# Optimization experiments

Hardware: AMD Instinct MI355X
Metric: run time of the kernel (lower is better)

Reference implementation:

```python
import jax, jax.numpy as jnp
import numpy as np

NEG = -1e30

def setup_inputs() -> dict:
    key = jax.random.key(0)
    k1, k2, k3, k4, k5 = jax.random.split(key, 5)
    B, N, M, D = 32, 2048, 512, 512
    C = jax.random.normal(k1, (B, N, D), dtype=jnp.float32)
    Q = jax.random.normal(k2, (B, M, D), dtype=jnp.float32)
    Cmask = jax.random.randint(k3, (B, N), 0, 2, dtype=jnp.int32)
    Qmask = jax.random.randint(k4, (B, M), 0, 2, dtype=jnp.int32)
    # Linear(3*dim, 1, bias=False) weight, flattened to a (3*dim,) vector.
    bound = 1.0 / np.sqrt(3 * D)
    w = jax.random.uniform(k5, (3 * D,), dtype=jnp.float32, minval=-bound, maxval=bound)
    return {"C": C, "Q": Q, "Cmask": Cmask, "Qmask": Qmask, "w": w}

def reference(C, Q, Cmask, Qmask, w):
    D = C.shape[-1]
    w1, w2, w3 = w[:D], w[D:2 * D], w[2 * D:]
    # Trilinear similarity, decomposed: S = w1.Ct + w2.Qt + w3.(Ct*Qt)
    S = (jnp.einsum('bnd,d->bn', C, w1)[:, :, None]
         + jnp.einsum('bmd,d->bm', Q, w2)[:, None, :]
         + jnp.einsum('bnd,bmd->bnm', C * w3, Q))  # [B, N, M]
    Qm = Qmask.astype(S.dtype)[:, None, :]  # [B, 1, M]; 1 = masked
    Cm = Cmask.astype(S.dtype)[:, :, None]  # [B, N, 1]
    S1 = jax.nn.softmax(S * (1.0 - Qm) + Qm * NEG, axis=2)
    S2 = jax.nn.softmax(S * (1.0 - Cm) + Cm * NEG, axis=1)
    A = jnp.einsum('bnm,bmd->bnd', S1, Q)
    T = jnp.einsum('bnm,bnd->bmd', S2, C)     # S2^T @ C
    Bout = jnp.einsum('bnm,bmd->bnd', S1, T)  # S1 @ (S2^T @ C)
    return (A, Bout)
```

## Files before the change

kernel.cpp:

```cpp
#include <hip/hip_runtime.h>

#define BB 32
#define NN 2048
#define MM 512
#define DD 512
#define TS 64
#define KC 16
#define PAD 4
#define LDKH 40

typedef _Float16 half4f __attribute__((ext_vector_type(4)));
typedef _Float16 half8f __attribute__((ext_vector_type(8)));
typedef float    f32x16 __attribute__((ext_vector_type(16)));

__global__ __launch_bounds__(256) void k_dots(const float* __restrict__ C, const float* __restrict__ Q,
                                              const float* __restrict__ w,
                                              float* __restrict__ c1, float* __restrict__ q2) {
    int wid  = blockIdx.x * 4 + (threadIdx.x >> 6);
    int lane = threadIdx.x & 63;
    const int NR1 = BB * NN;
    const float* src; const float* wv; float* dst;
    if (wid < NR1) { src = C + (size_t)wid * DD; wv = w;       dst = c1 + wid; }
    else { int r = wid - NR1; src = Q + (size_t)r * DD; wv = w + DD; dst = q2 + r; }
    float4 a0 = *(const float4*)(src + lane * 8);
    float4 a1 = *(const float4*)(src + lane * 8 + 4);
    float4 b0 = *(const float4*)(wv  + lane * 8);
    float4 b1 = *(const float4*)(wv  + lane * 8 + 4);
    float s = a0.x * b0.x + a0.y * b0.y + a0.z * b0.z + a0.w * b0.w
            + a1.x * b1.x + a1.y * b1.y + a1.z * b1.z + a1.w * b1.w;
#pragma unroll
    for (int o = 32; o > 0; o >>= 1) s += __shfl_down(s, o);
    if (lane == 0) *dst = s;
}

__global__ __launch_bounds__(256) void k_qt(const float* __restrict__ Q, const int* __restrict__ Qmask,
                                            _Float16* __restrict__ Qt) {
    __shared__ float Ls[64][65];
    const int bid = blockIdx.x;
    const int b   = bid >> 6;
    const int rem = bid & 63;
    const int m0  = (rem >> 3) << 6;
    const int d0  = (rem & 7) << 6;
    const int tid = threadIdx.x;
    const int r   = tid >> 4;
    const int c4  = (tid & 15) << 2;
#pragma unroll
    for (int p = 0; p < 4; ++p) {
        float4 v = *(const float4*)(Q + ((size_t)(b * MM + m0 + r + p * 16)) * DD + d0 + c4);
        const int m = r + p * 16;
        Ls[c4 + 0][m] = v.x; Ls[c4 + 1][m] = v.y; Ls[c4 + 2][m] = v.z; Ls[c4 + 3][m] = v.w;
    }
    __syncthreads();
    float z[4];
#pragma unroll
    for (int i = 0; i < 4; ++i) z[i] = Qmask[b * MM + m0 + c4 + i] ? 0.f : 1.f;
#pragma unroll
    for (int p = 0; p < 4; ++p) {
        const int d = r + p * 16;
        half4f o;
#pragma unroll
        for (int i = 0; i < 4; ++i) o[i] = (_Float16)(Ls[d][c4 + i] * z[i]);
        *(half4f*)&Qt[((size_t)(b * DD + d0 + d)) * MM + m0 + c4] = o;
    }
}

__global__ __launch_bounds__(256) void k_ct(const float* __restrict__ C, _Float16* __restrict__ Ct) {
    __shared__ float Ls[64][65];
    const int bid = blockIdx.x;
    const int b   = bid >> 8;
    const int nn0 = ((bid >> 3) & 31) << 6;
    const int dd0 = (bid & 7) << 6;
    const int tid = threadIdx.x;
    const int r   = tid >> 4;
    const int c4  = (tid & 15) << 2;
#pragma unroll
    for (int p = 0; p < 4; ++p) {
        const int n = r + (p << 4);
        float4 v = *(const float4*)(C + ((size_t)(b * NN + nn0 + n)) * DD + dd0 + c4);
        Ls[c4 + 0][n] = v.x; Ls[c4 + 1][n] = v.y; Ls[c4 + 2][n] = v.z; Ls[c4 + 3][n] = v.w;
    }
    __syncthreads();
#pragma unroll
    for (int p = 0; p < 4; ++p) {
        const int d = r + (p << 4);
        half4f o;
#pragma unroll
        for (int i = 0; i < 4; ++i) o[i] = (_Float16)Ls[d][c4 + i];
        *(half4f*)&Ct[((size_t)(b * DD + dd0 + d)) * NN + nn0 + c4] = o;
    }
}

__global__ __launch_bounds__(256) void k_te(const _Float16* __restrict__ E, const int* __restrict__ Cmask,
                                            _Float16* __restrict__ Et) {
    __shared__ float Ls[64][65];
    const int bid = blockIdx.x;
    const int b   = bid >> 8;
    const int nn0 = ((bid >> 3) & 31) << 6;
    const int mm0 = (bid & 7) << 6;
    const int tid = threadIdx.x;
    const int r   = tid >> 4;
    const int c4  = (tid & 15) << 2;
#pragma unroll
    for (int p = 0; p < 4; ++p) {
        const int n = r + (p << 4);
        half4f v = *(const half4f*)&E[((size_t)(b * NN + nn0 + n)) * MM + mm0 + c4];
        const float z = Cmask[b * NN + nn0 + n] ? 0.f : 1.f;
        Ls[c4 + 0][n] = (float)v[0] * z; Ls[c4 + 1][n] = (float)v[1] * z;
        Ls[c4 + 2][n] = (float)v[2] * z; Ls[c4 + 3][n] = (float)v[3] * z;
    }
    __syncthreads();
#pragma unroll
    for (int p = 0; p < 4; ++p) {
        const int m = r + (p << 4);
        half4f o;
#pragma unroll
        for (int i = 0; i < 4; ++i) o[i] = (_Float16)Ls[m][c4 + i];
        *(half4f*)&Et[((size_t)(b * MM + mm0 + m)) * NN + nn0 + c4] = o;
    }
}

__global__ __launch_bounds__(256, 2) void k_sgemm(const float* __restrict__ C, const float* __restrict__ Q,
                                                  const float* __restrict__ w,
                                                  const int* __restrict__ Cmask, const int* __restrict__ Qmask,
                                                  const float* __restrict__ c1, const float* __restrict__ q2,
                                                  _Float16* __restrict__ E, float* __restrict__ rsum,
                                                  float* __restrict__ csum) {
    __shared__ _Float16 Ah[128 * LDKH], Al[128 * LDKH], Bh[128 * LDKH], Bl[128 * LDKH];
    __shared__ float rowp[128], colp[128], cmz[128], qmz[128], c1s[128], q2s[128];
    const int hw  = blockIdx.x;
    const int bid = ((hw & 7) << 8) | (hw >> 3);
    const int b   = bid >> 6;
    const int rem = bid & 63;
    const int n0  = (rem >> 2) << 7;
    const int m0  = (rem & 3) << 7;
    const int tid = threadIdx.x;
    const int lane = tid & 63;
    const int wid  = tid >> 6;
    const int wr = wid >> 1, wc = wid & 1;
    const int srow = tid >> 3;
    const int sc4  = (tid & 7) << 2;
    if (tid < 128) {
        rowp[tid] = 0.f; colp[tid] = 0.f;
        cmz[tid] = Cmask[b * NN + n0 + tid] ? 0.f : 1.f;
        c1s[tid] = c1[b * NN + n0 + tid];
    } else {
        const int t = tid - 128;
        qmz[t] = Qmask[b * MM + m0 + t] ? 0.f : 1.f;
        q2s[t] = q2[b * MM + m0 + t];
    }
    f32x16 accH[2][2] = {};
    f32x16 accX[2][2] = {};
    const int ar  = wr * 64 + (lane & 31);
    const int bc  = wc * 64 + (lane & 31);
    const int kof = (lane >> 5) << 3;
    const float* Cb = C + ((size_t)(b * NN + n0)) * DD;
    const float* Qb = Q + ((size_t)(b * MM + m0)) * DD;
    const float* w3 = w + 2 * DD;
    for (int k0 = 0; k0 < DD; k0 += 32) {
        float4 wv = *(const float4*)(w3 + k0 + sc4);
        float4 ca[4], qa[4];
#pragma unroll
        for (int p = 0; p < 4; ++p) {
            ca[p] = *(const float4*)(Cb + (size_t)(srow + (p << 5)) * DD + k0 + sc4);
            qa[p] = *(const float4*)(Qb + (size_t)(srow + (p << 5)) * DD + k0 + sc4);
        }
        __syncthreads();
#pragma unroll
        for (int p = 0; p < 4; ++p) {
            const int ofs = (srow + (p << 5)) * LDKH + sc4;
            float ax[4] = {ca[p].x * wv.x, ca[p].y * wv.y, ca[p].z * wv.z, ca[p].w * wv.w};
            float bx[4] = {qa[p].x, qa[p].y, qa[p].z, qa[p].w};
            half4f ah, al, bh, bl;
#pragma unroll
            for (int e = 0; e < 4; ++e) {
                _Float16 h = (_Float16)ax[e]; ah[e] = h;
                al[e] = (_Float16)((ax[e] - (float)h) * 2048.f);
                _Float16 g = (_Float16)bx[e]; bh[e] = g;
                bl[e] = (_Float16)((bx[e] - (float)g) * 2048.f);
            }
            *(half4f*)&Ah[ofs] = ah; *(half4f*)&Al[ofs] = al;
            *(half4f*)&Bh[ofs] = bh; *(half4f*)&Bl[ofs] = bl;
        }
        __syncthreads();
#pragma unroll
        for (int h = 0; h < 2; ++h) {
            const int ko = (h << 4) + kof;
            half8f ah0 = *(const half8f*)&Ah[ar * LDKH + ko];
            half8f ah1 = *(const half8f*)&Ah[(ar + 32) * LDKH + ko];
            half8f al0 = *(const half8f*)&Al[ar * LDKH + ko];
            half8f al1 = *(const half8f*)&Al[(ar + 32) * LDKH + ko];
            half8f bh0 = *(const half8f*)&Bh[bc * LDKH + ko];
            half8f bh1 = *(const half8f*)&Bh[(bc + 32) * LDKH + ko];
            half8f bl0 = *(const half8f*)&Bl[bc * LDKH + ko];
            half8f bl1 = *(const half8f*)&Bl[(bc + 32) * LDKH + ko];
            accH[0][0] = __builtin_amdgcn_mfma_f32_32x32x16_f16(ah0, bh0, accH[0][0], 0, 0, 0);
            accH[0][1] = __builtin_amdgcn_mfma_f32_32x32x16_f16(ah0, bh1, accH[0][1], 0, 0, 0);
            accH[1][0] = __builtin_amdgcn_mfma_f32_32x32x16_f16(ah1, bh0, accH[1][0], 0, 0, 0);
            accH[1][1] = __builtin_amdgcn_mfma_f32_32x32x16_f16(ah1, bh1, accH[1][1], 0, 0, 0);
            accX[0][0] = __builtin_amdgcn_mfma_f32_32x32x16_f16(ah0, bl0, accX[0][0], 0, 0, 0);
            accX[0][0] = __builtin_amdgcn_mfma_f32_32x32x16_f16(al0, bh0, accX[0][0], 0, 0, 0);
            accX[0][1] = __builtin_amdgcn_mfma_f32_32x32x16_f16(ah0, bl1, accX[0][1], 0, 0, 0);
            accX[0][1] = __builtin_amdgcn_mfma_f32_32x32x16_f16(al0, bh1, accX[0][1], 0, 0, 0);
            accX[1][0] = __builtin_amdgcn_mfma_f32_32x32x16_f16(ah1, bl0, accX[1][0], 0, 0, 0);
            accX[1][0] = __builtin_amdgcn_mfma_f32_32x32x16_f16(al1, bh0, accX[1][0], 0, 0, 0);
            accX[1][1] = __builtin_amdgcn_mfma_f32_32x32x16_f16(ah1, bl1, accX[1][1], 0, 0, 0);
            accX[1][1] = __builtin_amdgcn_mfma_f32_32x32x16_f16(al1, bh1, accX[1][1], 0, 0, 0);
        }
    }
    const float inv2k = 4.8828125e-4f;
    const int mcol0 = wc * 64 + (lane & 31);
    const float qz0 = qmz[mcol0], qz1 = qmz[mcol0 + 32];
    const float q2v0 = q2s[mcol0], q2v1 = q2s[mcol0 + 32];
    const int hi4 = (lane >> 5) << 2;
    float colacc0 = 0.f, colacc1 = 0.f;
#pragma unroll
    for (int i = 0; i < 2; ++i) {
#pragma unroll
        for (int r = 0; r < 16; ++r) {
            const int nloc = wr * 64 + i * 32 + (r & 3) + ((r >> 2) << 3) + hi4;
            const float base = c1s[nloc];
            float S0 = accH[i][0][r] + accX[i][0][r] * inv2k + base + q2v0;
            float S1 = accH[i][1][r] + accX[i][1][r] * inv2k + base + q2v1;
            float e0 = __expf(S0), e1 = __expf(S1);
            _Float16 h0 = (_Float16)e0, h1 = (_Float16)e1;
            float eq0 = (float)h0, eq1 = (float)h1;
            const size_t erow = ((size_t)(b * NN + n0 + nloc)) * MM + m0;
            E[erow + mcol0]      = h0;
            E[erow + mcol0 + 32] = h1;
            const float cz = cmz[nloc];
            colacc0 += eq0 * cz;
            colacc1 += eq1 * cz;
            float rv = eq0 * qz0 + eq1 * qz1;
            rv += __shfl_xor(rv, 1);  rv += __shfl_xor(rv, 2);
            rv += __shfl_xor(rv, 4);  rv += __shfl_xor(rv, 8);
            rv += __shfl_xor(rv, 16);
            if ((lane & 31) == 0) atomicAdd(&rowp[nloc], rv);
        }
    }
    atomicAdd(&colp[mcol0], colacc0);
    atomicAdd(&colp[mcol0 + 32], colacc1);
    __syncthreads();
    if (tid < 128) atomicAdd(&rsum[b * NN + n0 + tid], rowp[tid]);
    else atomicAdd(&csum[b * MM + m0 + tid - 128], colp[tid - 128]);
}

__global__ __launch_bounds__(256, 2) void k_T(const _Float16* __restrict__ Ct,
                                              const _Float16* __restrict__ Et,
                                              const float* __restrict__ csum,
                                              const int* __restrict__ Qmask,
                                              _Float16* __restrict__ Tt) {
    __shared__ _Float16 As[128 * LDKH];
    __shared__ _Float16 Bs[128 * LDKH];
    const int hw  = blockIdx.x;
    const int bid = ((hw & 7) << 6) | (hw >> 3);
    const int b   = bid >> 4;
    const int rem = bid & 15;
    const int d0  = (rem >> 2) << 7;
    const int m0  = (rem & 3) << 7;
    const int tid = threadIdx.x;
    const int lane = tid & 63;
    const int wid  = tid >> 6;
    const int wr = wid >> 1, wc = wid & 1;
    const int srow = tid >> 2;
    const int scol = (tid & 3) << 3;
    const _Float16* g0 = Ct + ((size_t)(b * DD + d0 + srow)) * NN + scol;
    const _Float16* g1 = Et + ((size_t)(b * MM + m0 + srow)) * NN + scol;
    const int wofs = srow * LDKH + scol;
    f32x16 acc[2][2] = {};
    const int ar  = wr * 64 + (lane & 31);
    const int bc  = wc * 64 + (lane & 31);
    const int kof = (lane >> 5) << 3;
    for (int k0 = 0; k0 < NN; k0 += 32) {
        half8f a0v = *(const half8f*)(g0 + k0);
        half8f a1v = *(const half8f*)(g0 + k0 + (size_t)64 * NN);
        half8f b0v = *(const half8f*)(g1 + k0);
        half8f b1v = *(const half8f*)(g1 + k0 + (size_t)64 * NN);
        __syncthreads();
        *(half8f*)&As[wofs]             = a0v;
        *(half8f*)&As[wofs + 64 * LDKH] = a1v;
        *(half8f*)&Bs[wofs]             = b0v;
        *(half8f*)&Bs[wofs + 64 * LDKH] = b1v;
        __syncthreads();
#pragma unroll
        for (int h = 0; h < 2; ++h) {
            const int ko = (h << 4) + kof;
            half8f a0 = *(const half8f*)&As[ar * LDKH + ko];
            half8f a1 = *(const half8f*)&As[(ar + 32) * LDKH + ko];
            half8f b0 = *(const half8f*)&Bs[bc * LDKH + ko];
            half8f b1 = *(const half8f*)&Bs[(bc + 32) * LDKH + ko];
            acc[0][0] = __builtin_amdgcn_mfma_f32_32x32x16_f16(a0, b0, acc[0][0], 0, 0, 0);
            acc[0][1] = __builtin_amdgcn_mfma_f32_32x32x16_f16(a0, b1, acc[0][1], 0, 0, 0);
            acc[1][0] = __builtin_amdgcn_mfma_f32_32x32x16_f16(a1, b0, acc[1][0], 0, 0, 0);
            acc[1][1] = __builtin_amdgcn_mfma_f32_32x32x16_f16(a1, b1, acc[1][1], 0, 0, 0);
        }
    }
    const int mc0 = m0 + wc * 64 + (lane & 31);
    const float s0 = (Qmask[b * MM + mc0]      ? 0.f : 1.f) / csum[b * MM + mc0];
    const float s1 = (Qmask[b * MM + mc0 + 32] ? 0.f : 1.f) / csum[b * MM + mc0 + 32];
    const int hi4 = (lane >> 5) << 2;
#pragma unroll
    for (int i = 0; i < 2; ++i) {
#pragma unroll
        for (int r = 0; r < 16; ++r) {
            const int d = d0 + wr * 64 + i * 32 + (r & 3) + ((r >> 2) << 3) + hi4;
            const size_t o = ((size_t)(b * DD + d)) * MM + mc0;
            Tt[o]      = (_Float16)(acc[i][0][r] * s0);
            Tt[o + 32] = (_Float16)(acc[i][1][r] * s1);
        }
    }
}

#define KS 32

__global__ __launch_bounds__(256, 2) void k_AB(const _Float16* __restrict__ E,
                                               const _Float16* __restrict__ Qt,
                                               const _Float16* __restrict__ Tt,
                                               const float* __restrict__ rsum,
                                               float* __restrict__ outA, float* __restrict__ outB) {
    __shared__ _Float16 Es[128 * LDKH];
    __shared__ _Float16 Ws[2][128 * LDKH];
    const int hw  = blockIdx.x;
    const int bid = ((hw & 7) << 8) | (hw >> 3);
    const int b   = bid >> 6;
    const int rem = bid & 63;
    const int n0  = (rem >> 2) << 7;
    const int d0  = (rem & 3) << 7;
    const int tid = threadIdx.x;
    const int lane = tid & 63;
    const int wid  = tid >> 6;
    const int wr = wid >> 1, wc = wid & 1;
    const int srow = tid >> 2;
    const int scol = (tid & 3) << 3;
    const _Float16* g0 = E  + ((size_t)(b * NN + n0 + srow)) * MM + scol;
    const _Float16* g1 = Qt + ((size_t)(b * DD + d0 + srow)) * MM + scol;
    const _Float16* g2 = Tt + ((size_t)(b * DD + d0 + srow)) * MM + scol;
    const int wofs = srow * LDKH + scol;
    f32x16 accA[2][2] = {};
    f32x16 accB[2][2] = {};
    const int ar  = wr * 64 + (lane & 31);
    const int bc  = wc * 64 + (lane & 31);
    const int kof = (lane >> 5) << 3;
    for (int k0 = 0; k0 < MM; k0 += KS) {
        half8f e0 = *(const half8f*)(g0 + k0);
        half8f e1 = *(const half8f*)(g0 + k0 + (size_t)64 * MM);
        half8f q0 = *(const half8f*)(g1 + k0);
        half8f q1 = *(const half8f*)(g1 + k0 + (size_t)64 * MM);
        half8f t0 = *(const half8f*)(g2 + k0);
        half8f t1 = *(const half8f*)(g2 + k0 + (size_t)64 * MM);
        __syncthreads();
        *(half8f*)&Es[wofs]                = e0;
        *(half8f*)&Es[wofs + 64 * LDKH]    = e1;
        *(half8f*)&Ws[0][wofs]             = q0;
        *(half8f*)&Ws[0][wofs + 64 * LDKH] = q1;
        *(half8f*)&Ws[1][wofs]             = t0;
        *(half8f*)&Ws[1][wofs + 64 * LDKH] = t1;
        __syncthreads();
#pragma unroll
        for (int h = 0; h < 2; ++h) {
            const int ko = (h << 4) + kof;
            half8f a0  = *(const half8f*)&Es[ar * LDKH + ko];
            half8f a1  = *(const half8f*)&Es[(ar + 32) * LDKH + ko];
            half8f bq0 = *(const half8f*)&Ws[0][bc * LDKH + ko];
            half8f bq1 = *(const half8f*)&Ws[0][(bc + 32) * LDKH + ko];
            half8f bt0 = *(const half8f*)&Ws[1][bc * LDKH + ko];
            half8f bt1 = *(const half8f*)&Ws[1][(bc + 32) * LDKH + ko];
            accA[0][0] = __builtin_amdgcn_mfma_f32_32x32x16_f16(a0, bq0, accA[0][0], 0, 0, 0);
            accA[0][1] = __builtin_amdgcn_mfma_f32_32x32x16_f16(a0, bq1, accA[0][1], 0, 0, 0);
            accA[1][0] = __builtin_amdgcn_mfma_f32_32x32x16_f16(a1, bq0, accA[1][0], 0, 0, 0);
            accA[1][1] = __builtin_amdgcn_mfma_f32_32x32x16_f16(a1, bq1, accA[1][1], 0, 0, 0);
            accB[0][0] = __builtin_amdgcn_mfma_f32_32x32x16_f16(a0, bt0, accB[0][0], 0, 0, 0);
            accB[0][1] = __builtin_amdgcn_mfma_f32_32x32x16_f16(a0, bt1, accB[0][1], 0, 0, 0);
            accB[1][0] = __builtin_amdgcn_mfma_f32_32x32x16_f16(a1, bt0, accB[1][0], 0, 0, 0);
            accB[1][1] = __builtin_amdgcn_mfma_f32_32x32x16_f16(a1, bt1, accB[1][1], 0, 0, 0);
        }
    }
    const int dc = d0 + wc * 64 + (lane & 31);
#pragma unroll
    for (int i = 0; i < 2; ++i) {
#pragma unroll
        for (int r = 0; r < 16; ++r) {
            const int row = (r & 3) + ((r >> 2) << 3) + ((lane >> 5) << 2);
            const int n = n0 + wr * 64 + i * 32 + row;
            const float inv = __builtin_amdgcn_rcpf(rsum[b * NN + n]);
            const size_t o = ((size_t)(b * NN + n)) * DD + dc;
            outA[o]      = accA[i][0][r] * inv;
            outA[o + 32] = accA[i][1][r] * inv;
            outB[o]      = accB[i][0][r] * inv;
            outB[o + 32] = accB[i][1][r] * inv;
        }
    }
}

extern "C" void kernel_launch(void* const* d_in, const int* in_sizes, int n_in,
                              void* d_out, int out_size, void* d_ws, size_t ws_size,
                              hipStream_t stream) {
    const float* C = (const float*)d_in[0];
    const float* Q = (const float*)d_in[1];
    const int* Cmask = (const int*)d_in[2];
    const int* Qmask = (const int*)d_in[3];
    const float* w  = (const float*)d_in[4];

    const size_t BNM = (size_t)BB * NN * MM;
    const size_t BMD = (size_t)BB * MM * DD;
    const size_t BND = (size_t)BB * NN * DD;
    const size_t BN  = (size_t)BB * NN;
    const size_t BM  = (size_t)BB * MM;

    _Float16* E  = (_Float16*)d_ws;
    _Float16* Tt = E + BNM;
    _Float16* Qt = Tt + BMD;
    float* fbase = (float*)(Qt + BMD);
    float* c1   = fbase;
    float* q2   = c1 + BN;
    float* rsum = q2 + BM;
    float* csum = rsum + BN;

    _Float16* Ct = (_Float16*)d_out;
    _Float16* Et = (_Float16*)((float*)d_out + BND);

    hipMemsetAsync(rsum, 0, (BN + BM) * sizeof(float), stream);

    k_dots<<<(int)((BN + BM) / 4), 256, 0, stream>>>(C, Q, w, c1, q2);
    k_qt<<<BB * 64, 256, 0, stream>>>(Q, Qmask, Qt);
    k_ct<<<BB * 256, 256, 0, stream>>>(C, Ct);
    k_sgemm<<<2048, 256, 0, stream>>>(C, Q, w, Cmask, Qmask, c1, q2, E, rsum, csum);
    k_te<<<BB * 256, 256, 0, stream>>>(E, Cmask, Et);
    k_T<<<512, 256, 0, stream>>>(Ct, Et, csum, Qmask, Tt);
    k_AB<<<2048, 256, 0, stream>>>(E, Qt, Tt, rsum,
                                   (float*)d_out, (float*)d_out + BND);
}
```

Measured before the change: 755.7 us.

## Precompute fp16 hi/lo splits in prep kernels and register-prefetch GEMM tiles

```diff
diff --git a/kernel.cpp b/kernel.cpp
--- a/kernel.cpp
+++ b/kernel.cpp
@@ -4,10 +4,8 @@
 #define NN 2048
 #define MM 512
 #define DD 512
-#define TS 64
-#define KC 16
-#define PAD 4
 #define LDKH 40
+#define LDK64 72
 
 typedef _Float16 half4f __attribute__((ext_vector_type(4)));
 typedef _Float16 half8f __attribute__((ext_vector_type(8)));
@@ -33,8 +31,9 @@
     if (lane == 0) *dst = s;
 }
 
-__global__ __launch_bounds__(256) void k_qt(const float* __restrict__ Q, const int* __restrict__ Qmask,
-                                            _Float16* __restrict__ Qt) {
+__global__ __launch_bounds__(256) void k_prepQ(const float* __restrict__ Q, const int* __restrict__ Qmask,
+                                               _Float16* __restrict__ Qt,
+                                               _Float16* __restrict__ Qh, _Float16* __restrict__ Ql) {
     __shared__ float Ls[64][65];
     const int bid = blockIdx.x;
     const int b   = bid >> 6;
@@ -46,9 +45,18 @@
     const int c4  = (tid & 15) << 2;
 #pragma unroll
     for (int p = 0; p < 4; ++p) {
-        float4 v = *(const float4*)(Q + ((size_t)(b * MM + m0 + r + p * 16)) * DD + d0 + c4);
-        const int m = r + p * 16;
+        const int m = r + (p << 4);
+        const size_t o = ((size_t)(b * MM + m0 + m)) * DD + d0 + c4;
+        float4 v = *(const float4*)(Q + o);
         Ls[c4 + 0][m] = v.x; Ls[c4 + 1][m] = v.y; Ls[c4 + 2][m] = v.z; Ls[c4 + 3][m] = v.w;
+        half4f hh, ll;
+        float x0 = v.x, x1 = v.y, x2 = v.z, x3 = v.w;
+        hh[0] = (_Float16)x0; ll[0] = (_Float16)((x0 - (float)hh[0]) * 2048.f);
+        hh[1] = (_Float16)x1; ll[1] = (_Float16)((x1 - (float)hh[1]) * 2048.f);
+        hh[2] = (_Float16)x2; ll[2] = (_Float16)((x2 - (float)hh[2]) * 2048.f);
+        hh[3] = (_Float16)x3; ll[3] = (_Float16)((x3 - (float)hh[3]) * 2048.f);
+        *(half4f*)&Qh[o] = hh;
+        *(half4f*)&Ql[o] = ll;
     }
     __syncthreads();
     float z[4];
@@ -56,7 +64,7 @@
     for (int i = 0; i < 4; ++i) z[i] = Qmask[b * MM + m0 + c4 + i] ? 0.f : 1.f;
 #pragma unroll
     for (int p = 0; p < 4; ++p) {
-        const int d = r + p * 16;
+        const int d = r + (p << 4);
         half4f o;
 #pragma unroll
         for (int i = 0; i < 4; ++i) o[i] = (_Float16)(Ls[d][c4 + i] * z[i]);
@@ -64,7 +72,9 @@
     }
 }
 
-__global__ __launch_bounds__(256) void k_ct(const float* __restrict__ C, _Float16* __restrict__ Ct) {
+__global__ __launch_bounds__(256) void k_prepC(const float* __restrict__ C, const float* __restrict__ w,
+                                               _Float16* __restrict__ Ct,
+                                               _Float16* __restrict__ Ch, _Float16* __restrict__ Cl) {
     __shared__ float Ls[64][65];
     const int bid = blockIdx.x;
     const int b   = bid >> 8;
@@ -73,11 +83,22 @@
     const int tid = threadIdx.x;
     const int r   = tid >> 4;
     const int c4  = (tid & 15) << 2;
+    const float* w3 = w + 2 * DD;
+    const float4 wv = *(const float4*)(w3 + dd0 + c4);
 #pragma unroll
     for (int p = 0; p < 4; ++p) {
         const int n = r + (p << 4);
-        float4 v = *(const float4*)(C + ((size_t)(b * NN + nn0 + n)) * DD + dd0 + c4);
+        const size_t o = ((size_t)(b * NN + nn0 + n)) * DD + dd0 + c4;
+        float4 v = *(const float4*)(C + o);
         Ls[c4 + 0][n] = v.x; Ls[c4 + 1][n] = v.y; Ls[c4 + 2][n] = v.z; Ls[c4 + 3][n] = v.w;
+        float x0 = v.x * wv.x, x1 = v.y * wv.y, x2 = v.z * wv.z, x3 = v.w * wv.w;
+        half4f hh, ll;
+        hh[0] = (_Float16)x0; ll[0] = (_Float16)((x0 - (float)hh[0]) * 2048.f);
+        hh[1] = (_Float16)x1; ll[1] = (_Float16)((x1 - (float)hh[1]) * 2048.f);
+        hh[2] = (_Float16)x2; ll[2] = (_Float16)((x2 - (float)hh[2]) * 2048.f);
+        hh[3] = (_Float16)x3; ll[3] = (_Float16)((x3 - (float)hh[3]) * 2048.f);
+        *(half4f*)&Ch[o] = hh;
+        *(half4f*)&Cl[o] = ll;
     }
     __syncthreads();
 #pragma unroll
@@ -119,13 +140,13 @@
     }
 }
 
-__global__ __launch_bounds__(256, 2) void k_sgemm(const float* __restrict__ C, const float* __restrict__ Q,
-                                                  const float* __restrict__ w,
+__global__ __launch_bounds__(256, 2) void k_sgemm(const _Float16* __restrict__ Ch, const _Float16* __restrict__ Cl,
+                                                  const _Float16* __restrict__ Qh, const _Float16* __restrict__ Ql,
                                                   const int* __restrict__ Cmask, const int* __restrict__ Qmask,
                                                   const float* __restrict__ c1, const float* __restrict__ q2,
                                                   _Float16* __restrict__ E, float* __restrict__ rsum,
                                                   float* __restrict__ csum) {
-    __shared__ _Float16 Ah[128 * LDKH], Al[128 * LDKH], Bh[128 * LDKH], Bl[128 * LDKH];
+    __shared__ _Float16 sAh[128 * LDKH], sAl[128 * LDKH], sBh[128 * LDKH], sBl[128 * LDKH];
     __shared__ float rowp[128], colp[128], cmz[128], qmz[128], c1s[128], q2s[128];
     const int hw  = blockIdx.x;
     const int bid = ((hw & 7) << 8) | (hw >> 3);
@@ -137,8 +158,8 @@
     const int lane = tid & 63;
     const int wid  = tid >> 6;
     const int wr = wid >> 1, wc = wid & 1;
-    const int srow = tid >> 3;
-    const int sc4  = (tid & 7) << 2;
+    const int srow = tid >> 2;
+    const int sseg = (tid & 3) << 3;
     if (tid < 128) {
         rowp[tid] = 0.f; colp[tid] = 0.f;
         cmz[tid] = Cmask[b * NN + n0 + tid] ? 0.f : 1.f;
@@ -148,51 +169,54 @@
         qmz[t] = Qmask[b * MM + m0 + t] ? 0.f : 1.f;
         q2s[t] = q2[b * MM + m0 + t];
     }
+    const _Float16* gAh = Ch + ((size_t)(b * NN + n0 + srow)) * DD + sseg;
+    const _Float16* gAl = Cl + ((size_t)(b * NN + n0 + srow)) * DD + sseg;
+    const _Float16* gBh = Qh + ((size_t)(b * MM + m0 + srow)) * DD + sseg;
+    const _Float16* gBl = Ql + ((size_t)(b * MM + m0 + srow)) * DD + sseg;
+    const int wofs0 = srow * LDKH + sseg;
+    const int wofs1 = (srow + 64) * LDKH + sseg;
+    half8f pah0 = *(const half8f*)(gAh);
+    half8f pah1 = *(const half8f*)(gAh + (size_t)64 * DD);
+    half8f pal0 = *(const half8f*)(gAl);
+    half8f pal1 = *(const half8f*)(gAl + (size_t)64 * DD);
+    half8f pbh0 = *(const half8f*)(gBh);
+    half8f pbh1 = *(const half8f*)(gBh + (size_t)64 * DD);
+    half8f pbl0 = *(const half8f*)(gBl);
+    half8f pbl1 = *(const half8f*)(gBl + (size_t)64 * DD);
     f32x16 accH[2][2] = {};
     f32x16 accX[2][2] = {};
     const int ar  = wr * 64 + (lane & 31);
     const int bc  = wc * 64 + (lane & 31);
     const int kof = (lane >> 5) << 3;
-    const float* Cb = C + ((size_t)(b * NN + n0)) * DD;
-    const float* Qb = Q + ((size_t)(b * MM + m0)) * DD;
-    const float* w3 = w + 2 * DD;
-    for (int k0 = 0; k0 < DD; k0 += 32) {
-        float4 wv = *(const float4*)(w3 + k0 + sc4);
-        float4 ca[4], qa[4];
-#pragma unroll
-        for (int p = 0; p < 4; ++p) {
-            ca[p] = *(const float4*)(Cb + (size_t)(srow + (p << 5)) * DD + k0 + sc4);
-            qa[p] = *(const float4*)(Qb + (size_t)(srow + (p << 5)) * DD + k0 + sc4);
-        }
-        __syncthreads();
-#pragma unroll
-        for (int p = 0; p < 4; ++p) {
-            const int ofs = (srow + (p << 5)) * LDKH + sc4;
-            float ax[4] = {ca[p].x * wv.x, ca[p].y * wv.y, ca[p].z * wv.z, ca[p].w * wv.w};
-            float bx[4] = {qa[p].x, qa[p].y, qa[p].z, qa[p].w};
-            half4f ah, al, bh, bl;
-#pragma unroll
-            for (int e = 0; e < 4; ++e) {
-                _Float16 h = (_Float16)ax[e]; ah[e] = h;
-                al[e] = (_Float16)((ax[e] - (float)h) * 2048.f);
-                _Float16 g = (_Float16)bx[e]; bh[e] = g;
-                bl[e] = (_Float16)((bx[e] - (float)g) * 2048.f);
-            }
-            *(half4f*)&Ah[ofs] = ah; *(half4f*)&Al[ofs] = al;
-            *(half4f*)&Bh[ofs] = bh; *(half4f*)&Bl[ofs] = bl;
-        }
-        __syncthreads();
+    for (int it = 0; it < 16; ++it) {
+        __syncthreads();
+        *(half8f*)&sAh[wofs0] = pah0; *(half8f*)&sAh[wofs1] = pah1;
+        *(half8f*)&sAl[wofs0] = pal0; *(half8f*)&sAl[wofs1] = pal1;
+        *(half8f*)&sBh[wofs0] = pbh0; *(half8f*)&sBh[wofs1] = pbh1;
+        *(half8f*)&sBl[wofs0] = pbl0; *(half8f*)&sBl[wofs1] = pbl1;
+        __syncthreads();
+        if (it < 15) {
+            const int k0 = (it + 1) << 5;
+            pah0 = *(const half8f*)(gAh + k0);
+            pah1 = *(const half8f*)(gAh + k0 + (size_t)64 * DD);
+            pal0 = *(const half8f*)(gAl + k0);
+            pal1 = *(const half8f*)(gAl + k0 + (size_t)64 * DD);
+            pbh0 = *(const half8f*)(gBh + k0);
+            pbh1 = *(const half8f*)(gBh + k0 + (size_t)64 * DD);
+            pbl0 = *(const half8f*)(gBl + k0);
+            pbl1 = *(const half8f*)(gBl + k0 + (size_t)64 * DD);
+        }
 #pragma unroll
         for (int h = 0; h < 2; ++h) {
             const int ko = (h << 4) + kof;
-            half8f ah0 = *(const half8f*)&Ah[ar * LDKH + ko];
-            half8f ah1 = *(const half8f*)&Ah[(ar + 32) * LDKH + ko];
-            half8f al0 = *(const half8f*)&Al[ar * LDKH + ko];
-            half8f al1 = *(const half8f*)&Al[(ar + 32) * LDKH + ko];
-            half8f bh0 = *(const half8f*)&Bh[bc * LDKH + ko];
-            half8f bh1 = *(const half8f*)&Bh[(bc + 32) * LDKH + ko];
-            half8f bl0 = *(const half8f*)&Bl[bc * LDKH + ko];
-            half8f bl1 = *(const half8f*)&Bl[(bc + 32) * LDKH + ko];
+            half8f ah0 = *(const half8f*)&sAh[ar * LDKH + ko];
+            half8f ah1 = *(const half8f*)&sAh[(ar + 32) * LDKH + ko];
+            half8f al0 = *(const half8f*)&sAl[ar * LDKH + ko];
+            half8f al1 = *(const half8f*)&sAl[(ar + 32) * LDKH + ko];
+            half8f bh0 = *(const half8f*)&sBh[bc * LDKH + ko];
+            half8f bh1 = *(const half8f*)&sBh[(bc + 32) * LDKH + ko];
+            half8f bl0 = *(const half8f*)&sBl[bc * LDKH + ko];
+            half8f bl1 = *(const half8f*)&sBl[(bc + 32) * LDKH + ko];
             accH[0][0] = __builtin_amdgcn_mfma_f32_32x32x16_f16(ah0, bh0, accH[0][0], 0, 0, 0);
             accH[0][1] = __builtin_amdgcn_mfma_f32_32x32x16_f16(ah0, bh1, accH[0][1], 0, 0, 0);
             accH[1][0] = __builtin_amdgcn_mfma_f32_32x32x16_f16(ah1, bh0, accH[1][0], 0, 0, 0);
@@ -244,13 +268,13 @@
     else atomicAdd(&csum[b * MM + m0 + tid - 128], colp[tid - 128]);
 }
 
-__global__ __launch_bounds__(256, 2) void k_T(const _Float16* __restrict__ Ct,
+__global__ __launch_bounds__(256, 3) void k_T(const _Float16* __restrict__ Ct,
                                               const _Float16* __restrict__ Et,
                                               const float* __restrict__ csum,
                                               const int* __restrict__ Qmask,
                                               _Float16* __restrict__ Tt) {
-    __shared__ _Float16 As[128 * LDKH];
-    __shared__ _Float16 Bs[128 * LDKH];
+    __shared__ _Float16 As[128 * LDK64];
+    __shared__ _Float16 Bs[128 * LDK64];
     const int hw  = blockIdx.x;
     const int bid = ((hw & 7) << 6) | (hw >> 3);
     const int b   = bid >> 4;
@@ -261,33 +285,44 @@
     const int lane = tid & 63;
     const int wid  = tid >> 6;
     const int wr = wid >> 1, wc = wid & 1;
-    const int srow = tid >> 2;
-    const int scol = (tid & 3) << 3;
-    const _Float16* g0 = Ct + ((size_t)(b * DD + d0 + srow)) * NN + scol;
-    const _Float16* g1 = Et + ((size_t)(b * MM + m0 + srow)) * NN + scol;
-    const int wofs = srow * LDKH + scol;
+    const int srow = tid >> 3;
+    const int sseg = (tid & 7) << 3;
+    const _Float16* g0 = Ct + ((size_t)(b * DD + d0 + srow)) * NN + sseg;
+    const _Float16* g1 = Et + ((size_t)(b * MM + m0 + srow)) * NN + sseg;
+    const int wofs = srow * LDK64 + sseg;
+    half8f pa[4], pb[4];
+#pragma unroll
+    for (int p = 0; p < 4; ++p) {
+        pa[p] = *(const half8f*)(g0 + (size_t)(p * 32) * NN);
+        pb[p] = *(const half8f*)(g1 + (size_t)(p * 32) * NN);
+    }
     f32x16 acc[2][2] = {};
     const int ar  = wr * 64 + (lane & 31);
     const int bc  = wc * 64 + (lane & 31);
     const int kof = (lane >> 5) << 3;
-    for (int k0 = 0; k0 < NN; k0 += 32) {
-        half8f a0v = *(const half8f*)(g0 + k0);
-        half8f a1v = *(const half8f*)(g0 + k0 + (size_t)64 * NN);
-        half8f b0v = *(const half8f*)(g1 + k0);
-        half8f b1v = *(const half8f*)(g1 + k0 + (size_t)64 * NN);
-        __syncthreads();
-        *(half8f*)&As[wofs]             = a0v;
-        *(half8f*)&As[wofs + 64 * LDKH] = a1v;
-        *(half8f*)&Bs[wofs]             = b0v;
-        *(half8f*)&Bs[wofs + 64 * LDKH] = b1v;
-        __syncthreads();
-#pragma unroll
-        for (int h = 0; h < 2; ++h) {
+    for (int it = 0; it < 32; ++it) {
+        __syncthreads();
+#pragma unroll
+        for (int p = 0; p < 4; ++p) {
+            *(half8f*)&As[wofs + p * 32 * LDK64] = pa[p];
+            *(half8f*)&Bs[wofs + p * 32 * LDK64] = pb[p];
+        }
+        __syncthreads();
+        if (it < 31) {
+            const int k0 = (it + 1) << 6;
+#pragma unroll
+            for (int p = 0; p < 4; ++p) {
+                pa[p] = *(const half8f*)(g0 + (size_t)(p * 32) * NN + k0);
+                pb[p] = *(const half8f*)(g1 + (size_t)(p * 32) * NN + k0);
+            }
+        }
+#pragma unroll
+        for (int h = 0; h < 4; ++h) {
             const int ko = (h << 4) + kof;
-            half8f a0 = *(const half8f*)&As[ar * LDKH + ko];
-            half8f a1 = *(const half8f*)&As[(ar + 32) * LDKH + ko];
-            half8f b0 = *(const half8f*)&Bs[bc * LDKH + ko];
-            half8f b1 = *(const half8f*)&Bs[(bc + 32) * LDKH + ko];
+            half8f a0 = *(const half8f*)&As[ar * LDK64 + ko];
+            half8f a1 = *(const half8f*)&As[(ar + 32) * LDK64 + ko];
+            half8f b0 = *(const half8f*)&Bs[bc * LDK64 + ko];
+            half8f b1 = *(const half8f*)&Bs[(bc + 32) * LDK64 + ko];
             acc[0][0] = __builtin_amdgcn_mfma_f32_32x32x16_f16(a0, b0, acc[0][0], 0, 0, 0);
             acc[0][1] = __builtin_amdgcn_mfma_f32_32x32x16_f16(a0, b1, acc[0][1], 0, 0, 0);
             acc[1][0] = __builtin_amdgcn_mfma_f32_32x32x16_f16(a1, b0, acc[1][0], 0, 0, 0);
@@ -310,15 +345,13 @@
     }
 }
 
-#define KS 32
-
 __global__ __launch_bounds__(256, 2) void k_AB(const _Float16* __restrict__ E,
                                                const _Float16* __restrict__ Qt,
                                                const _Float16* __restrict__ Tt,
                                                const float* __restrict__ rsum,
                                                float* __restrict__ outA, float* __restrict__ outB) {
-    __shared__ _Float16 Es[128 * LDKH];
-    __shared__ _Float16 Ws[2][128 * LDKH];
+    __shared__ _Float16 Es[128 * LDK64];
+    __shared__ _Float16 Ws[2][128 * LDK64];
     const int hw  = blockIdx.x;
     const int bid = ((hw & 7) << 8) | (hw >> 3);
     const int b   = bid >> 6;
@@ -329,41 +362,51 @@
     const int lane = tid & 63;
     const int wid  = tid >> 6;
     const int wr = wid >> 1, wc = wid & 1;
-    const int srow = tid >> 2;
-    const int scol = (tid & 3) << 3;
-    const _Float16* g0 = E  + ((size_t)(b * NN + n0 + srow)) * MM + scol;
-    const _Float16* g1 = Qt + ((size_t)(b * DD + d0 + srow)) * MM + scol;
-    const _Float16* g2 = Tt + ((size_t)(b * DD + d0 + srow)) * MM + scol;
-    const int wofs = srow * LDKH + scol;
+    const int srow = tid >> 3;
+    const int sseg = (tid & 7) << 3;
+    const _Float16* g0 = E  + ((size_t)(b * NN + n0 + srow)) * MM + sseg;
+    const _Float16* g1 = Qt + ((size_t)(b * DD + d0 + srow)) * MM + sseg;
+    const _Float16* g2 = Tt + ((size_t)(b * DD + d0 + srow)) * MM + sseg;
+    const int wofs = srow * LDK64 + sseg;
+    half8f pe[4], pq[4], pt[4];
+#pragma unroll
+    for (int p = 0; p < 4; ++p) {
+        pe[p] = *(const half8f*)(g0 + (size_t)(p * 32) * MM);
+        pq[p] = *(const half8f*)(g1 + (size_t)(p * 32) * MM);
+        pt[p] = *(const half8f*)(g2 + (size_t)(p * 32) * MM);
+    }
     f32x16 accA[2][2] = {};
     f32x16 accB[2][2] = {};
     const int ar  = wr * 64 + (lane & 31);
     const int bc  = wc * 64 + (lane & 31);
     const int kof = (lane >> 5) << 3;
-    for (int k0 = 0; k0 < MM; k0 += KS) {
-        half8f e0 = *(const half8f*)(g0 + k0);
-        half8f e1 = *(const half8f*)(g0 + k0 + (size_t)64 * MM);
-        half8f q0 = *(const half8f*)(g1 + k0);
-        half8f q1 = *(const half8f*)(g1 + k0 + (size_t)64 * MM);
-        half8f t0 = *(const half8f*)(g2 + k0);
-        half8f t1 = *(const half8f*)(g2 + k0 + (size_t)64 * MM);
-        __syncthreads();
-        *(half8f*)&Es[wofs]                = e0;
-        *(half8f*)&Es[wofs + 64 * LDKH]    = e1;
-        *(half8f*)&Ws[0][wofs]             = q0;
-        *(half8f*)&Ws[0][wofs + 64 * LDKH] = q1;
-        *(half8f*)&Ws[1][wofs]             = t0;
-        *(half8f*)&Ws[1][wofs + 64 * LDKH] = t1;
-        __syncthreads();
-#pragma unroll
-        for (int h = 0; h < 2; ++h) {
+    for (int it = 0; it < 8; ++it) {
+        __syncthreads();
+#pragma unroll
+        for (int p = 0; p < 4; ++p) {
+            *(half8f*)&Es[wofs + p * 32 * LDK64]    = pe[p];
+            *(half8f*)&Ws[0][wofs + p * 32 * LDK64] = pq[p];
+            *(half8f*)&Ws[1][wofs + p * 32 * LDK64] = pt[p];
+        }
+        __syncthreads();
+        if (it < 7) {
+            const int k0 = (it + 1) << 6;
+#pragma unroll
+            for (int p = 0; p < 4; ++p) {
+                pe[p] = *(const half8f*)(g0 + (size_t)(p * 32) * MM + k0);
+                pq[p] = *(const half8f*)(g1 + (size_t)(p * 32) * MM + k0);
+                pt[p] = *(const half8f*)(g2 + (size_t)(p * 32) * MM + k0);
+            }
+        }
+#pragma unroll
+        for (int h = 0; h < 4; ++h) {
             const int ko = (h << 4) + kof;
-            half8f a0  = *(const half8f*)&Es[ar * LDKH + ko];
-            half8f a1  = *(const half8f*)&Es[(ar + 32) * LDKH + ko];
-            half8f bq0 = *(const half8f*)&Ws[0][bc * LDKH + ko];
-            half8f bq1 = *(const half8f*)&Ws[0][(bc + 32) * LDKH + ko];
-            half8f bt0 = *(const half8f*)&Ws[1][bc * LDKH + ko];
-            half8f bt1 = *(const half8f*)&Ws[1][(bc + 32) * LDKH + ko];
+            half8f a0  = *(const half8f*)&Es[ar * LDK64 + ko];
+            half8f a1  = *(const half8f*)&Es[(ar + 32) * LDK64 + ko];
+            half8f bq0 = *(const half8f*)&Ws[0][bc * LDK64 + ko];
+            half8f bq1 = *(const half8f*)&Ws[0][(bc + 32) * LDK64 + ko];
+            half8f bt0 = *(const half8f*)&Ws[1][bc * LDK64 + ko];
+            half8f bt1 = *(const half8f*)&Ws[1][(bc + 32) * LDK64 + ko];
             accA[0][0] = __builtin_amdgcn_mfma_f32_32x32x16_f16(a0, bq0, accA[0][0], 0, 0, 0);
             accA[0][1] = __builtin_amdgcn_mfma_f32_32x32x16_f16(a0, bq1, accA[0][1], 0, 0, 0);
             accA[1][0] = __builtin_amdgcn_mfma_f32_32x32x16_f16(a1, bq0, accA[1][0], 0, 0, 0);
@@ -416,14 +459,18 @@
     float* csum = rsum + BN;
 
     _Float16* Ct = (_Float16*)d_out;
-    _Float16* Et = (_Float16*)((float*)d_out + BND);
+    _Float16* Ch = Ct + BND;
+    _Float16* Cl = Ch + BND;
+    _Float16* Qh = Cl + BND;
+    _Float16* Ql = Qh + BMD;
+    _Float16* Et = Ch;
 
     hipMemsetAsync(rsum, 0, (BN + BM) * sizeof(float), stream);
 
     k_dots<<<(int)((BN + BM) / 4), 256, 0, stream>>>(C, Q, w, c1, q2);
-    k_qt<<<BB * 64, 256, 0, stream>>>(Q, Qmask, Qt);
-    k_ct<<<BB * 256, 256, 0, stream>>>(C, Ct);
-    k_sgemm<<<2048, 256, 0, stream>>>(C, Q, w, Cmask, Qmask, c1, q2, E, rsum, csum);
+    k_prepQ<<<BB * 64, 256, 0, stream>>>(Q, Qmask, Qt, Qh, Ql);
+    k_prepC<<<BB * 256, 256, 0, stream>>>(C, w, Ct, Ch, Cl);
+    k_sgemm<<<2048, 256, 0, stream>>>(Ch, Cl, Qh, Ql, Cmask, Qmask, c1, q2, E, rsum, csum);
     k_te<<<BB * 256, 256, 0, stream>>>(E, Cmask, Et);
     k_T<<<512, 256, 0, stream>>>(Ct, Et, csum, Qmask, Tt);
     k_AB<<<2048, 256, 0, stream>>>(E, Qt, Tt, rsum,
```

Result: no change. 767.1 us (+1.5%).
